# Optimization experiments

Hardware: AMD Instinct MI355X
Metric: run time of the kernel (lower is better)

The kernel has to match this reference:

```python
import jax, jax.numpy as jnp
import numpy as np

B, T, D, H, NH, E, K = 8, 1024, 512, 2048, 8, 8, 31
LN_EPS = 1e-12  # espnet LayerNorm default
BN_EPS = 1e-5


def setup_inputs() -> dict:
    key = jax.random.key(0)
    ks = iter(jax.random.split(key, 64))
    nrm = lambda shape, s=0.02: jax.random.normal(next(ks), shape, jnp.float32) * s
    return dict(
        x=jax.random.normal(next(ks), (B, T, D), jnp.float32),
        mask=jnp.ones((B, 1, T), bool),
        dialectid=jax.random.randint(next(ks), (B,), 1, E + 1),  # 1-based dialect ids
        ln_ffmac_g=jnp.ones((D,), jnp.float32), ln_ffmac_b=jnp.zeros((D,), jnp.float32),
        w1_mac=nrm((D, H)), b1_mac=jnp.zeros((H,), jnp.float32),
        w2_mac=nrm((H, D)), b2_mac=jnp.zeros((D,), jnp.float32),
        ln_mha_g=jnp.ones((D,), jnp.float32), ln_mha_b=jnp.zeros((D,), jnp.float32),
        wq=nrm((D, D)), bq=jnp.zeros((D,), jnp.float32),
        wk=nrm((D, D)), bk=jnp.zeros((D,), jnp.float32),
        wv=nrm((D, D)), bv=jnp.zeros((D,), jnp.float32),
        wo=nrm((D, D)), bo=jnp.zeros((D,), jnp.float32),
        ln_conv_g=jnp.ones((D,), jnp.float32), ln_conv_b=jnp.zeros((D,), jnp.float32),
        pw1_w=nrm((D, 2 * D)), pw1_b=jnp.zeros((2 * D,), jnp.float32),
        dw_w=nrm((D, 1, K)), dw_b=jnp.zeros((D,), jnp.float32),
        bn_g=jnp.ones((D,), jnp.float32), bn_b=jnp.zeros((D,), jnp.float32),
        bn_mean=jnp.zeros((D,), jnp.float32), bn_var=jnp.ones((D,), jnp.float32),
        pw2_w=nrm((D, D)), pw2_b=jnp.zeros((D,), jnp.float32),
        ln_ff_g=jnp.ones((D,), jnp.float32), ln_ff_b=jnp.zeros((D,), jnp.float32),
        gate_w=nrm((D, E)), gate_b=jnp.zeros((E,), jnp.float32),
        e_w1=nrm((E, D, H)), e_b1=jnp.zeros((E, H), jnp.float32),
        e_w2=nrm((E, H, D)), e_b2=jnp.zeros((E, D), jnp.float32),
        ln_final_g=jnp.ones((D,), jnp.float32), ln_final_b=jnp.zeros((D,), jnp.float32),
    )


def layer_norm(h, g, b):
    m = h.mean(-1, keepdims=True)
    v = ((h - m) ** 2).mean(-1, keepdims=True)
    return (h - m) * jax.lax.rsqrt(v + LN_EPS) * g + b


def mha(x, mask, wq, bq, wk, bk, wv, bv, wo, bo):
    dk = D // NH
    q = (x @ wq + bq).reshape(B, T, NH, dk)
    k = (x @ wk + bk).reshape(B, T, NH, dk)
    v = (x @ wv + bv).reshape(B, T, NH, dk)
    scores = jnp.einsum('bqhd,bkhd->bhqk', q, k) / jnp.sqrt(jnp.float32(dk))
    scores = jnp.where(mask[:, None, :, :], scores, jnp.float32(-1e9))  # [B,1,1,T] bcast
    attn = jax.nn.softmax(scores, axis=-1)
    o = jnp.einsum('bhqk,bkhd->bqhd', attn, v).reshape(B, T, D)
    return o @ wo + bo


def conv_module(x, pw1_w, pw1_b, dw_w, dw_b, bn_g, bn_b, bn_mean, bn_var, pw2_w, pw2_b):
    h = x @ pw1_w + pw1_b                                  # [B,T,2D]
    a, g = jnp.split(h, 2, axis=-1)
    h = a * jax.nn.sigmoid(g)                              # GLU -> [B,T,D]
    hc = jnp.transpose(h, (0, 2, 1))                       # [B,D,T]
    hc = jax.lax.conv_general_dilated(
        hc, dw_w, window_strides=(1,), padding=[(K // 2, K // 2)],
        dimension_numbers=('NCH', 'OIH', 'NCH'), feature_group_count=D)
    hc = hc + dw_b[None, :, None]
    h = jnp.transpose(hc, (0, 2, 1))                       # [B,T,D]
    h = (h - bn_mean) * jax.lax.rsqrt(bn_var + BN_EPS) * bn_g + bn_b  # BatchNorm (eval)
    h = h * jax.nn.sigmoid(h)                              # Swish
    return h @ pw2_w + pw2_b


def moe_ff(x, dialectid, gate_w, gate_b, e_w1, e_b1, e_w2, e_b2):
    probs = jax.nn.softmax(x.mean(1) @ gate_w + gate_b, axis=-1)   # [B,E]
    chosen = jnp.clip(dialectid - 1, 0, E - 1)                     # custom_expert_chosen
    w1 = e_w1[chosen]; b1 = e_b1[chosen]                           # gather [B,D,H]
    w2 = e_w2[chosen]; b2 = e_b2[chosen]
    h = jax.nn.relu(jnp.einsum('btd,bdh->bth', x, w1) + b1[:, None, :])
    y = jnp.einsum('bth,bhd->btd', h, w2) + b2[:, None, :]
    return y, probs, chosen


def reference(x, mask, dialectid,
              ln_ffmac_g, ln_ffmac_b, w1_mac, b1_mac, w2_mac, b2_mac,
              ln_mha_g, ln_mha_b, wq, bq, wk, bk, wv, bv, wo, bo,
              ln_conv_g, ln_conv_b, pw1_w, pw1_b, dw_w, dw_b,
              bn_g, bn_b, bn_mean, bn_var, pw2_w, pw2_b,
              ln_ff_g, ln_ff_b, gate_w, gate_b, e_w1, e_b1, e_w2, e_b2,
              ln_final_g, ln_final_b):
    ff_scale = 0.5  # macaron present
    # macaron feed-forward (pre-norm)
    residual = x
    h = layer_norm(x, ln_ffmac_g, ln_ffmac_b)
    h = jax.nn.relu(h @ w1_mac + b1_mac) @ w2_mac + b2_mac
    x = residual + ff_scale * h
    # self-attention
    residual = x
    h = layer_norm(x, ln_mha_g, ln_mha_b)
    x = residual + mha(h, mask, wq, bq, wk, bk, wv, bv, wo, bo)
    # convolution module
    residual = x
    h = layer_norm(x, ln_conv_g, ln_conv_b)
    x = residual + conv_module(h, pw1_w, pw1_b, dw_w, dw_b, bn_g, bn_b, bn_mean, bn_var, pw2_w, pw2_b)
    # MoE feed-forward
    residual = x
    h = layer_norm(x, ln_ff_g, ln_ff_b)
    h, expert_probs, expert_chosen = moe_ff(h, dialectid, gate_w, gate_b, e_w1, e_b1, e_w2, e_b2)
    x = residual + ff_scale * h
    # final norm (conv module present)
    x = layer_norm(x, ln_final_g, ln_final_b)
    return x
```

## Files before the change

### kernel.cpp

```cpp
#include <hip/hip_runtime.h>
#include <hip/hip_bf16.h>

constexpr int Bc = 8, Tc = 1024, Dc = 512, Hc = 2048, NHc = 8, DKc = 64, KC = 31;
constexpr long NTD = (long)Bc * Tc * Dc;

typedef short  bf16x8 __attribute__((ext_vector_type(8)));
typedef float  f32x4  __attribute__((ext_vector_type(4)));

__device__ __forceinline__ float bf2f(unsigned short u) {
  union { unsigned int i; float f; } c; c.i = ((unsigned int)u) << 16; return c.f;
}
__device__ __forceinline__ unsigned short f2bf(float f) {
  union { float f; unsigned int i; } c; c.f = f;
  unsigned int r = c.i + 0x7FFFu + ((c.i >> 16) & 1u);
  return (unsigned short)(r >> 16);
}
__device__ __forceinline__ float ldsc(const void* p, long i, int isbf) {
  return isbf ? bf2f(((const unsigned short*)p)[i]) : ((const float*)p)[i];
}
__device__ __forceinline__ void gl_lds16(const unsigned short* g, unsigned short* l) {
  __builtin_amdgcn_global_load_lds((const __attribute__((address_space(1))) void*)g,
                                   (__attribute__((address_space(3))) void*)l, 16, 0, 0);
}

__global__ void detect_k(const unsigned int* __restrict__ g, int* __restrict__ flag) {
  if (threadIdx.x == 0) flag[0] = (g[0] == 0x3F803F80u) ? 1 : 0;
}

__global__ __launch_bounds__(256) void cvt_k(const void* __restrict__ x,
                                             float* __restrict__ y, int n,
                                             const int* __restrict__ flag) {
  int isbf = flag[0];
  int i = blockIdx.x * 256 + threadIdx.x;
  if (i < n) y[i] = ldsc(x, i, isbf);
}

__global__ __launch_bounds__(256) void packb_k(const void* __restrict__ bq,
    const void* __restrict__ bk, const void* __restrict__ bv,
    float* __restrict__ o, const int* __restrict__ flag) {
  int isbf = flag[0];
  int i = blockIdx.x * 256 + threadIdx.x;
  const void* p = (i < 512) ? bq : ((i < 1024) ? bk : bv);
  o[i] = ldsc(p, i & 511, isbf);
}

__global__ __launch_bounds__(256) void transpose_k(const void* __restrict__ src_,
    unsigned short* __restrict__ dst, int K, int N,
    const int* __restrict__ dialectid, int batch0, const int* __restrict__ flag)
{
  int isbf = flag[0];
  long sofs = 0;
  if (dialectid) {
    int ex = dialectid[batch0 + blockIdx.z] - 1;
    ex = ex < 0 ? 0 : (ex > 7 ? 7 : ex);
    sofs = (long)ex * K * N;
    dst += (long)blockIdx.z * K * N;
  }
  __shared__ unsigned short t[32][36];
  int k0 = blockIdx.y * 32, n0 = blockIdx.x * 32;
  int r = threadIdx.x >> 3, c4 = (threadIdx.x & 7) * 4;
  long si = sofs + (long)(k0 + r) * N + n0 + c4;
  if (isbf) {
    ushort4 v = *reinterpret_cast<const ushort4*>((const unsigned short*)src_ + si);
    t[r][c4] = v.x; t[r][c4 + 1] = v.y; t[r][c4 + 2] = v.z; t[r][c4 + 3] = v.w;
  } else {
    float4 f = *reinterpret_cast<const float4*>((const float*)src_ + si);
    t[r][c4] = f2bf(f.x); t[r][c4 + 1] = f2bf(f.y);
    t[r][c4 + 2] = f2bf(f.z); t[r][c4 + 3] = f2bf(f.w);
  }
  __syncthreads();
  ushort4 o;
  o.x = t[c4 + 0][r]; o.y = t[c4 + 1][r]; o.z = t[c4 + 2][r]; o.w = t[c4 + 3][r];
  *reinterpret_cast<ushort4*>(dst + (long)(n0 + r) * K + k0 + c4) = o;
}

__global__ __launch_bounds__(256) void ln_k(const float* __restrict__ src,
    const void* __restrict__ g, const void* __restrict__ b,
    unsigned short* __restrict__ dst, const int* __restrict__ flag)
{
  int isbf = flag[0];
  int row = blockIdx.x;
  const float* p = src + (long)row * Dc;
  int tid = threadIdx.x;
  float x0 = p[tid], x1 = p[tid + 256];
  float s = x0 + x1, ss = x0 * x0 + x1 * x1;
#pragma unroll
  for (int off = 32; off; off >>= 1) { s += __shfl_xor(s, off); ss += __shfl_xor(ss, off); }
  __shared__ float rs[4], rss[4];
  int wave = tid >> 6, lane = tid & 63;
  if (lane == 0) { rs[wave] = s; rss[wave] = ss; }
  __syncthreads();
  s = rs[0] + rs[1] + rs[2] + rs[3];
  ss = rss[0] + rss[1] + rss[2] + rss[3];
  float mean = s * (1.0f / Dc);
  float var  = ss * (1.0f / Dc) - mean * mean;
  float inv  = rsqrtf(fmaxf(var, 0.0f) + 1e-12f);
  long base = (long)row * Dc;
  dst[base + tid]       = f2bf((x0 - mean) * inv * ldsc(g, tid, isbf)       + ldsc(b, tid, isbf));
  dst[base + tid + 256] = f2bf((x1 - mean) * inv * ldsc(g, tid + 256, isbf) + ldsc(b, tid + 256, isbf));
}

template<bool FINAL>
__global__ __launch_bounds__(256) void redln_k(float* x,
    const unsigned short* pb, long pplane, float scale,
    const void* __restrict__ g, const void* __restrict__ b,
    void* dst, const int* __restrict__ flag)
{
  int isbf = flag[0];
  int row = blockIdx.x;
  int tid = threadIdx.x;
  long base = (long)row * Dc;
  float x0 = x[base + tid]       + scale * (bf2f(pb[base + tid])       + bf2f(pb[pplane + base + tid]));
  float x1 = x[base + tid + 256] + scale * (bf2f(pb[base + tid + 256]) + bf2f(pb[pplane + base + tid + 256]));
  if (!FINAL) { x[base + tid] = x0; x[base + tid + 256] = x1; }
  float s = x0 + x1, ss = x0 * x0 + x1 * x1;
#pragma unroll
  for (int off = 32; off; off >>= 1) { s += __shfl_xor(s, off); ss += __shfl_xor(ss, off); }
  __shared__ float rs[4], rss[4];
  int wave = tid >> 6, lane = tid & 63;
  if (lane == 0) { rs[wave] = s; rss[wave] = ss; }
  __syncthreads();
  s = rs[0] + rs[1] + rs[2] + rs[3];
  ss = rss[0] + rss[1] + rss[2] + rss[3];
  float mean = s * (1.0f / Dc);
  float var  = ss * (1.0f / Dc) - mean * mean;
  float inv  = rsqrtf(fmaxf(var, 0.0f) + 1e-12f);
  float o0 = (x0 - mean) * inv * ldsc(g, tid, isbf)       + ldsc(b, tid, isbf);
  float o1 = (x1 - mean) * inv * ldsc(g, tid + 256, isbf) + ldsc(b, tid + 256, isbf);
  if (FINAL && !isbf) {
    ((float*)dst)[base + tid]       = o0;
    ((float*)dst)[base + tid + 256] = o1;
  } else {
    ((unsigned short*)dst)[base + tid]       = f2bf(o0);
    ((unsigned short*)dst)[base + tid + 256] = f2bf(o1);
  }
}

constexpr int EPI_STORE = 0, EPI_RELU = 1, EPI_ADD = 2, EPI_ADDHALF = 3,
              EPI_ROWDK = 4, EPI_DKROW = 5, EPI_ROWDK_Q = 6, EPI_QKV = 7,
              EPI_PART = 8;

template<int EPI, bool MOE, int SPLITK>
__global__ __launch_bounds__(256) void mgemm_k(
    const unsigned short* __restrict__ A,
    const unsigned short* __restrict__ BT,
    const void* __restrict__ bias,
    void* __restrict__ dst,
    int Kd, int N, const int* __restrict__ dialectid, int row_base,
    const int* __restrict__ flag, long pplane)
{
  int isbf = flag[0];
  __shared__ unsigned short As[3][128 * 32];
  __shared__ unsigned short Bs[3][128 * 32];
  int row0 = blockIdx.x * 128;
  int col0 = blockIdx.y * 128;
  const unsigned short* Bp = BT;
  long bofs = 0;
  if (MOE) {
    int bb = (row_base + row0) >> 10;
    int ex = dialectid[bb] - 1; ex = ex < 0 ? 0 : (ex > 7 ? 7 : ex);
    Bp += (long)(bb & 3) * (long)Kd * N;
    bofs = (long)ex * N;
  }
  int tid = threadIdx.x;
  int lane = tid & 63, wave = tid >> 6;
  int wm = (wave >> 1) * 64, wn = (wave & 1) * 64;
  int lm = lane & 15, quad = lane >> 4;
  int acol = ((lane & 3) ^ ((lane >> 3) & 3)) * 8;
  int rsl = (quad ^ ((lm >> 1) & 3)) * 8;

  f32x4 acc[4][4];
#pragma unroll
  for (int i = 0; i < 4; ++i)
#pragma unroll
    for (int j = 0; j < 4; ++j) acc[i][j] = (f32x4){0.f, 0.f, 0.f, 0.f};

  int kslice = Kd / SPLITK;
  int kbeg = (SPLITK > 1) ? (int)blockIdx.z * kslice : 0;
  int kend = kbeg + kslice;

  auto stage = [&](int buf, int k0) {
#pragma unroll
    for (int j = 0; j < 2; ++j) {
      int seg = wave * 2 + j;
      int r = seg * 16 + (lane >> 2);
      gl_lds16(A  + (long)(row0 + r) * Kd + k0 + acol, As[buf] + seg * 512);
      gl_lds16(Bp + (long)(col0 + r) * Kd + k0 + acol, Bs[buf] + seg * 512);
    }
  };

  stage(0, kbeg);
  if (kbeg + 32 < kend) {
    stage(1, kbeg + 32);
    asm volatile("s_waitcnt vmcnt(4)" ::: "memory");
  } else {
    asm volatile("s_waitcnt vmcnt(0)" ::: "memory");
  }
  __builtin_amdgcn_s_barrier();

  int cur = 0;
  for (int k0 = kbeg; k0 < kend; k0 += 32) {
    int pf = (k0 + 64 < kend);
    if (pf) {
      int nb = cur + 2; if (nb >= 3) nb -= 3;
      stage(nb, k0 + 64);
    }
    bf16x8 af[4], bfr[4];
#pragma unroll
    for (int t = 0; t < 4; ++t) {
      af[t]  = *reinterpret_cast<const bf16x8*>(As[cur] + (wm + t * 16 + lm) * 32 + rsl);
      bfr[t] = *reinterpret_cast<const bf16x8*>(Bs[cur] + (wn + t * 16 + lm) * 32 + rsl);
    }
    __builtin_amdgcn_s_setprio(1);
#pragma unroll
    for (int mt = 0; mt < 4; ++mt)
#pragma unroll
      for (int nt = 0; nt < 4; ++nt)
        acc[mt][nt] = __builtin_amdgcn_mfma_f32_16x16x32_bf16(af[mt], bfr[nt], acc[mt][nt], 0, 0, 0);
    __builtin_amdgcn_s_setprio(0);
    if (pf) asm volatile("s_waitcnt vmcnt(4)" ::: "memory");
    else    asm volatile("s_waitcnt vmcnt(0)" ::: "memory");
    __builtin_amdgcn_s_barrier();
    ++cur; if (cur >= 3) cur -= 3;
  }

  long zofs = (EPI == EPI_PART) ? (long)blockIdx.z * pplane : 0;
#pragma unroll
  for (int mt = 0; mt < 4; ++mt) {
#pragma unroll
    for (int nt = 0; nt < 4; ++nt) {
      int n = col0 + wn + nt * 16 + lm;
      float bv = (EPI == EPI_QKV) ? ((const float*)bias)[n]
                                  : ldsc(bias, bofs + n, isbf);
      if (SPLITK > 1 && blockIdx.z != 0) bv = 0.0f;
#pragma unroll
      for (int r = 0; r < 4; ++r) {
        int m = row0 + wm + mt * 16 + quad * 4 + r;
        float v = acc[mt][nt][r] + bv;
        if (EPI == EPI_STORE)
          ((unsigned short*)dst)[(long)m * N + n] = f2bf(v);
        else if (EPI == EPI_RELU)
          ((unsigned short*)dst)[(long)m * N + n] = f2bf(fmaxf(v, 0.0f));
        else if (EPI == EPI_PART)
          ((unsigned short*)dst)[zofs + (long)(row_base + m) * N + n] = f2bf(v);
        else if (EPI == EPI_ADD) {
          if (SPLITK == 1) ((float*)dst)[(long)m * N + n] += v;
          else             atomicAdd((float*)dst + ((long)m * N + n), v);
        } else if (EPI == EPI_ADDHALF) {
          if (SPLITK == 1) ((float*)dst)[(long)m * N + n] += 0.5f * v;
          else             atomicAdd((float*)dst + ((long)m * N + n), 0.5f * v);
        } else if (EPI == EPI_QKV) {
          int which = n >> 9, d = n & 511, hh = d >> 6, dd = d & 63;
          int bb = m >> 10, t = m & 1023;
          unsigned short* o = (unsigned short*)dst;
          if (which == 0)
            o[((long)(bb * NHc + hh) * Tc + t) * DKc + dd] = f2bf(v * 0.125f);
          else if (which == 1)
            o[4194304 + ((long)(bb * NHc + hh) * Tc + t) * DKc + dd] = f2bf(v);
          else
            o[8388608 + ((long)(bb * NHc + hh) * DKc + dd) * Tc + t] = f2bf(v);
        } else {
          int bb = m >> 10, t = m & 1023, hh = n >> 6, dd = n & 63;
          if (EPI == EPI_ROWDK)
            ((unsigned short*)dst)[((long)(bb * NHc + hh) * Tc + t) * DKc + dd] = f2bf(v);
          else if (EPI == EPI_ROWDK_Q)
            ((unsigned short*)dst)[((long)(bb * NHc + hh) * Tc + t) * DKc + dd] = f2bf(v * 0.125f);
          else
            ((unsigned short*)dst)[((long)(bb * NHc + hh) * DKc + dd) * Tc + t] = f2bf(v);
        }
      }
    }
  }
}

__global__ __launch_bounds__(256) void fattn_k(const unsigned short* __restrict__ q,
    const unsigned short* __restrict__ k, const unsigned short* __restrict__ vT,
    unsigned short* __restrict__ out)
{
  constexpr int PST = 72;
  __shared__ unsigned short ks[64 * PST];
  __shared__ unsigned short vs[64 * PST];
  __shared__ unsigned short plds[4][16][PST];
  int tid = threadIdx.x;
  int lane = tid & 63, wave = tid >> 6;
  int lm = lane & 15, quad = lane >> 4;
  int bh = blockIdx.y;
  int trow0 = blockIdx.x * 64 + wave * 16;
  long qbase = (long)bh * Tc * DKc;
  long vbase = (long)bh * DKc * Tc;

  int srow = tid >> 2, sseg = (tid & 3) * 16;

  bf16x8 aq[2];
#pragma unroll
  for (int s = 0; s < 2; ++s)
    aq[s] = *reinterpret_cast<const bf16x8*>(q + qbase + (long)(trow0 + lm) * DKc + s * 32 + quad * 8);

  f32x4 acc_o[4];
#pragma unroll
  for (int nt = 0; nt < 4; ++nt) acc_o[nt] = (f32x4){0.f, 0.f, 0.f, 0.f};
  float lsum[4] = {0.f, 0.f, 0.f, 0.f};

  float4 kr0 = *reinterpret_cast<const float4*>(k  + qbase + (long)srow * DKc + sseg);
  float4 kr1 = *reinterpret_cast<const float4*>(k  + qbase + (long)srow * DKc + sseg + 8);
  float4 vr0 = *reinterpret_cast<const float4*>(vT + vbase + (long)srow * Tc + sseg);
  float4 vr1 = *reinterpret_cast<const float4*>(vT + vbase + (long)srow * Tc + sseg + 8);

  for (int kt = 0; kt < Tc; kt += 64) {
    __syncthreads();
    *reinterpret_cast<float4*>(&ks[srow * PST + sseg])     = kr0;
    *reinterpret_cast<float4*>(&ks[srow * PST + sseg + 8]) = kr1;
    *reinterpret_cast<float4*>(&vs[srow * PST + sseg])     = vr0;
    *reinterpret_cast<float4*>(&vs[srow * PST + sseg + 8]) = vr1;
    __syncthreads();
    if (kt + 64 < Tc) {
      int kn = kt + 64;
      kr0 = *reinterpret_cast<const float4*>(k  + qbase + (long)(kn + srow) * DKc + sseg);
      kr1 = *reinterpret_cast<const float4*>(k  + qbase + (long)(kn + srow) * DKc + sseg + 8);
      vr0 = *reinterpret_cast<const float4*>(vT + vbase + (long)srow * Tc + kn + sseg);
      vr1 = *reinterpret_cast<const float4*>(vT + vbase + (long)srow * Tc + kn + sseg + 8);
    }
    f32x4 accs[4];
#pragma unroll
    for (int nt = 0; nt < 4; ++nt) accs[nt] = (f32x4){0.f, 0.f, 0.f, 0.f};
#pragma unroll
    for (int s = 0; s < 2; ++s) {
#pragma unroll
      for (int nt = 0; nt < 4; ++nt) {
        bf16x8 bk = *reinterpret_cast<const bf16x8*>(&ks[(nt * 16 + lm) * PST + s * 32 + quad * 8]);
        accs[nt] = __builtin_amdgcn_mfma_f32_16x16x32_bf16(aq[s], bk, accs[nt], 0, 0, 0);
      }
    }
#pragma unroll
    for (int nt = 0; nt < 4; ++nt) {
#pragma unroll
      for (int r = 0; r < 4; ++r) {
        float p = __expf(accs[nt][r]);
        lsum[r] += p;
        plds[wave][quad * 4 + r][nt * 16 + lm] = f2bf(p);
      }
    }
#pragma unroll
    for (int s = 0; s < 2; ++s) {
      bf16x8 ap = *reinterpret_cast<const bf16x8*>(&plds[wave][lm][s * 32 + quad * 8]);
#pragma unroll
      for (int nt = 0; nt < 4; ++nt) {
        bf16x8 bv = *reinterpret_cast<const bf16x8*>(&vs[(nt * 16 + lm) * PST + s * 32 + quad * 8]);
        acc_o[nt] = __builtin_amdgcn_mfma_f32_16x16x32_bf16(ap, bv, acc_o[nt], 0, 0, 0);
      }
    }
  }
  int bb = bh >> 3, hh = bh & 7;
#pragma unroll
  for (int r = 0; r < 4; ++r) {
    float l = lsum[r];
    l += __shfl_xor(l, 1);
    l += __shfl_xor(l, 2);
    l += __shfl_xor(l, 4);
    l += __shfl_xor(l, 8);
    float inv = 1.0f / l;
    int t = trow0 + quad * 4 + r;
#pragma unroll
    for (int nt = 0; nt < 4; ++nt)
      out[((long)(bb * Tc + t)) * Dc + hh * DKc + nt * 16 + lm] = f2bf(acc_o[nt][r] * inv);
  }
}

__global__ __launch_bounds__(256) void glu_k(const unsigned short* __restrict__ h,
                                             unsigned short* __restrict__ o) {
  int i = blockIdx.x * 256 + threadIdx.x;
  int m = i >> 9, d = i & 511;
  float a = bf2f(h[(long)m * 1024 + d]);
  float g = bf2f(h[(long)m * 1024 + 512 + d]);
  o[i] = f2bf(a * (1.0f / (1.0f + expf(-g))));
}

constexpr int TT = 16;
__global__ __launch_bounds__(256) void dwconv_k(const unsigned short* __restrict__ src,
    const void* __restrict__ w,  const void* __restrict__ wb,
    const void* __restrict__ bng, const void* __restrict__ bnb,
    const void* __restrict__ bnm, const void* __restrict__ bnv,
    unsigned short* __restrict__ dst, const int* __restrict__ flag)
{
  int isbf = flag[0];
  long i = (long)blockIdx.x * 256 + threadIdx.x;
  int d  = (int)(i & 511);
  int tc = (int)((i >> 9) & 63);
  int b  = (int)(i >> 15);
  int t0 = tc * TT;
  const unsigned short* s = src + (long)b * Tc * Dc + d;

  float win[TT + KC - 1];
#pragma unroll
  for (int j = 0; j < TT + KC - 1; ++j) {
    int tt = t0 + j - 15;
    win[j] = ((unsigned)tt < (unsigned)Tc) ? bf2f(s[(long)tt * Dc]) : 0.0f;
  }
  float wreg[KC];
#pragma unroll
  for (int kk = 0; kk < KC; ++kk) wreg[kk] = ldsc(w, d * KC + kk, isbf);

  float bias  = ldsc(wb, d, isbf);
  float scale = ldsc(bng, d, isbf) * rsqrtf(ldsc(bnv, d, isbf) + 1e-5f);
  float bnmv  = ldsc(bnm, d, isbf);
  float bnbv  = ldsc(bnb, d, isbf);
  unsigned short* o = dst + (long)b * Tc * Dc + (long)t0 * Dc + d;
#pragma unroll
  for (int r = 0; r < TT; ++r) {
    float acc = bias;
#pragma unroll
    for (int kk = 0; kk < KC; ++kk) acc += win[r + kk] * wreg[kk];
    float v = (acc - bnmv) * scale + bnbv;
    v = v * (1.0f / (1.0f + expf(-v)));
    o[(long)r * Dc] = f2bf(v);
  }
}

extern "C" void kernel_launch(void* const* d_in, const int* in_sizes, int n_in,
                              void* d_out, int out_size, void* d_ws, size_t ws_size,
                              hipStream_t stream) {
  const int* dialectid = (const int*)d_in[2];
  auto P = [&](int i) { return (const void*)d_in[i]; };

  char* base = (char*)d_ws;
  float*          x_cur = (float*)base;
  unsigned short* hn    = (unsigned short*)(base + (16L << 20));
  unsigned short* wt    = (unsigned short*)(base + (24L << 20));
  unsigned short* wtmoe = (unsigned short*)(base + (32L << 20));
  unsigned short* hidF  = (unsigned short*)(base + (32L << 20));
  unsigned short* dyn   = (unsigned short*)(base + (48L << 20));
  int*            flag  = (int*)(base + (72L << 20));
  unsigned short* w1T  = wt;
  unsigned short* w2T  = wt + 1048576;
  unsigned short* wqT  = wt + 2097152;
  unsigned short* wkT  = wt + 2359296;
  unsigned short* wvT  = wt + 2621440;
  unsigned short* woT  = wt + 2883584;
  unsigned short* pw1T = wt + 3145728;
  unsigned short* pw2T = wt + 3670016;
  float*          qkvb = (float*)(wt + 3932160);

  unsigned short* pbMac = hn;
  const long      ppMac = 25165824;
  unsigned short* pbDyn = dyn;
  const long      ppDyn = 4194304;
  unsigned short* pbMoE = wt;
  const long      ppMoE = 20971520;

  dim3 blk(256);
  const int nElem = (int)NTD;

  detect_k<<<1, 64, 0, stream>>>((const unsigned int*)d_in[3], flag);
  cvt_k<<<nElem / 256, blk, 0, stream>>>(P(0), x_cur, nElem, flag);

  transpose_k<<<dim3(64, 16), blk, 0, stream>>>(P(5),  w1T,  512, 2048, nullptr, 0, flag);
  transpose_k<<<dim3(16, 64), blk, 0, stream>>>(P(7),  w2T,  2048, 512, nullptr, 0, flag);
  transpose_k<<<dim3(16, 16), blk, 0, stream>>>(P(11), wqT,  512, 512,  nullptr, 0, flag);
  transpose_k<<<dim3(16, 16), blk, 0, stream>>>(P(13), wkT,  512, 512,  nullptr, 0, flag);
  transpose_k<<<dim3(16, 16), blk, 0, stream>>>(P(15), wvT,  512, 512,  nullptr, 0, flag);
  transpose_k<<<dim3(16, 16), blk, 0, stream>>>(P(17), woT,  512, 512,  nullptr, 0, flag);
  transpose_k<<<dim3(32, 16), blk, 0, stream>>>(P(21), pw1T, 512, 1024, nullptr, 0, flag);
  transpose_k<<<dim3(16, 16), blk, 0, stream>>>(P(29), pw2T, 512, 512,  nullptr, 0, flag);
  packb_k<<<6, blk, 0, stream>>>(P(12), P(14), P(16), qkvb, flag);

  unsigned short* hid = dyn;
  unsigned short* qb  = dyn;
  unsigned short* kb  = dyn + 4194304;
  unsigned short* vb  = dyn + 8388608;
  unsigned short* pw1o = dyn;
  unsigned short* gluo = dyn + 8388608;

  ln_k<<<Bc * Tc, blk, 0, stream>>>(x_cur, P(3), P(4), hn, flag);
  mgemm_k<EPI_RELU, false, 1><<<dim3(64, 16), blk, 0, stream>>>(
      hn, w1T, P(6), hidF, 512, 2048, nullptr, 0, flag, 0L);
  mgemm_k<EPI_PART, false, 2><<<dim3(64, 4, 2), blk, 0, stream>>>(
      hidF, w2T, P(8), pbMac, 2048, 512, nullptr, 0, flag, ppMac);
  redln_k<false><<<Bc * Tc, blk, 0, stream>>>(x_cur, pbMac, ppMac, 0.5f, P(9), P(10), hn, flag);

  mgemm_k<EPI_QKV, false, 1><<<dim3(64, 12), blk, 0, stream>>>(
      hn, wqT, qkvb, qb, 512, 1536, nullptr, 0, flag, 0L);
  fattn_k<<<dim3(Tc / 64, Bc * NHc), blk, 0, stream>>>(qb, kb, vb, hn);
  mgemm_k<EPI_PART, false, 2><<<dim3(64, 4, 2), blk, 0, stream>>>(
      hn, woT, P(18), pbDyn, 512, 512, nullptr, 0, flag, ppDyn);
  redln_k<false><<<Bc * Tc, blk, 0, stream>>>(x_cur, pbDyn, ppDyn, 1.0f, P(19), P(20), hn, flag);

  mgemm_k<EPI_STORE, false, 1><<<dim3(64, 8), blk, 0, stream>>>(hn, pw1T, P(22), pw1o, 512, 1024, nullptr, 0, flag, 0L);
  glu_k<<<nElem / 256, blk, 0, stream>>>(pw1o, gluo);
  dwconv_k<<<(int)(NTD / TT / 256), blk, 0, stream>>>(gluo, P(23), P(24), P(25), P(26), P(27), P(28), hn, flag);
  mgemm_k<EPI_PART, false, 2><<<dim3(64, 4, 2), blk, 0, stream>>>(
      hn, pw2T, P(30), pbDyn, 512, 512, nullptr, 0, flag, ppDyn);
  redln_k<false><<<Bc * Tc, blk, 0, stream>>>(x_cur, pbDyn, ppDyn, 1.0f, P(31), P(32), hn, flag);

  for (int c = 0; c < 2; ++c) {
    unsigned short* w1m = wtmoe;
    unsigned short* w2m = wtmoe + 4 * 1048576;
    transpose_k<<<dim3(64, 16, 4), blk, 0, stream>>>(P(35), w1m, 512, 2048, dialectid, c * 4, flag);
    transpose_k<<<dim3(16, 64, 4), blk, 0, stream>>>(P(37), w2m, 2048, 512, dialectid, c * 4, flag);
    mgemm_k<EPI_RELU, true, 1><<<dim3(32, 16), blk, 0, stream>>>(
        hn + (long)c * 4096 * 512, w1m, P(36), hid, 512, 2048, dialectid, c * 4096, flag, 0L);
    mgemm_k<EPI_PART, true, 2><<<dim3(32, 4, 2), blk, 0, stream>>>(
        hid, w2m, P(38), pbMoE, 2048, 512, dialectid, c * 4096, flag, ppMoE);
  }

  redln_k<true><<<Bc * Tc, blk, 0, stream>>>(x_cur, pbMoE, ppMoE, 0.5f, P(39), P(40), d_out, flag);
}
```

Baseline: 598.4 us.

## Process 32 query rows per wave in attention to reuse K/V tiles

Each wave in the attention kernel now handles two 16-row query tiles instead of one, so a block covers 128 query rows and every K/V tile staged in LDS feeds twice as many MFMAs. The grid shrinks from 1024 to 512 blocks and is flattened with a swizzle that places the 8 heads of one batch in consecutive block IDs. This halves K/V global loads and LDS staging per query row, but doubles accumulator registers and the P scratch buffer, which may reduce occupancy and leave fewer blocks to spread across CUs.

```diff
diff --git a/kernel.cpp b/kernel.cpp
--- a/kernel.cpp
+++ b/kernel.cpp
@@ -280,26 +280,33 @@
   constexpr int PST = 72;
   __shared__ unsigned short ks[64 * PST];
   __shared__ unsigned short vs[64 * PST];
-  __shared__ unsigned short plds[4][16][PST];
+  __shared__ unsigned short plds[4][32][PST];
   int tid = threadIdx.x;
   int lane = tid & 63, wave = tid >> 6;
   int lm = lane & 15, quad = lane >> 4;
-  int bh = blockIdx.y;
-  int trow0 = blockIdx.x * 64 + wave * 16;
+  int flat = blockIdx.x;
+  int bh = ((flat >> 6) << 3) | (flat & 7);
+  int qt = (flat >> 3) & 7;
+  int trow0 = qt * 128 + wave * 32;
   long qbase = (long)bh * Tc * DKc;
   long vbase = (long)bh * DKc * Tc;
 
   int srow = tid >> 2, sseg = (tid & 3) * 16;
 
-  bf16x8 aq[2];
-#pragma unroll
-  for (int s = 0; s < 2; ++s)
-    aq[s] = *reinterpret_cast<const bf16x8*>(q + qbase + (long)(trow0 + lm) * DKc + s * 32 + quad * 8);
-
-  f32x4 acc_o[4];
-#pragma unroll
-  for (int nt = 0; nt < 4; ++nt) acc_o[nt] = (f32x4){0.f, 0.f, 0.f, 0.f};
-  float lsum[4] = {0.f, 0.f, 0.f, 0.f};
+  bf16x8 aq[2][2];
+#pragma unroll
+  for (int mt = 0; mt < 2; ++mt)
+#pragma unroll
+    for (int s = 0; s < 2; ++s)
+      aq[mt][s] = *reinterpret_cast<const bf16x8*>(
+          q + qbase + (long)(trow0 + mt * 16 + lm) * DKc + s * 32 + quad * 8);
+
+  f32x4 acc_o[2][4];
+#pragma unroll
+  for (int mt = 0; mt < 2; ++mt)
+#pragma unroll
+    for (int nt = 0; nt < 4; ++nt) acc_o[mt][nt] = (f32x4){0.f, 0.f, 0.f, 0.f};
+  float lsum[2][4] = {{0.f, 0.f, 0.f, 0.f}, {0.f, 0.f, 0.f, 0.f}};
 
   float4 kr0 = *reinterpret_cast<const float4*>(k  + qbase + (long)srow * DKc + sseg);
   float4 kr1 = *reinterpret_cast<const float4*>(k  + qbase + (long)srow * DKc + sseg + 8);
@@ -320,49 +327,60 @@
       vr0 = *reinterpret_cast<const float4*>(vT + vbase + (long)srow * Tc + kn + sseg);
       vr1 = *reinterpret_cast<const float4*>(vT + vbase + (long)srow * Tc + kn + sseg + 8);
     }
-    f32x4 accs[4];
-#pragma unroll
-    for (int nt = 0; nt < 4; ++nt) accs[nt] = (f32x4){0.f, 0.f, 0.f, 0.f};
+    f32x4 accs[2][4];
+#pragma unroll
+    for (int mt = 0; mt < 2; ++mt)
+#pragma unroll
+      for (int nt = 0; nt < 4; ++nt) accs[mt][nt] = (f32x4){0.f, 0.f, 0.f, 0.f};
 #pragma unroll
     for (int s = 0; s < 2; ++s) {
 #pragma unroll
       for (int nt = 0; nt < 4; ++nt) {
         bf16x8 bk = *reinterpret_cast<const bf16x8*>(&ks[(nt * 16 + lm) * PST + s * 32 + quad * 8]);
-        accs[nt] = __builtin_amdgcn_mfma_f32_16x16x32_bf16(aq[s], bk, accs[nt], 0, 0, 0);
+#pragma unroll
+        for (int mt = 0; mt < 2; ++mt)
+          accs[mt][nt] = __builtin_amdgcn_mfma_f32_16x16x32_bf16(aq[mt][s], bk, accs[mt][nt], 0, 0, 0);
       }
     }
 #pragma unroll
-    for (int nt = 0; nt < 4; ++nt) {
-#pragma unroll
-      for (int r = 0; r < 4; ++r) {
-        float p = __expf(accs[nt][r]);
-        lsum[r] += p;
-        plds[wave][quad * 4 + r][nt * 16 + lm] = f2bf(p);
+    for (int mt = 0; mt < 2; ++mt)
+#pragma unroll
+      for (int nt = 0; nt < 4; ++nt) {
+#pragma unroll
+        for (int r = 0; r < 4; ++r) {
+          float p = __expf(accs[mt][nt][r]);
+          lsum[mt][r] += p;
+          plds[wave][mt * 16 + quad * 4 + r][nt * 16 + lm] = f2bf(p);
+        }
       }
-    }
 #pragma unroll
     for (int s = 0; s < 2; ++s) {
-      bf16x8 ap = *reinterpret_cast<const bf16x8*>(&plds[wave][lm][s * 32 + quad * 8]);
+      bf16x8 ap0 = *reinterpret_cast<const bf16x8*>(&plds[wave][lm][s * 32 + quad * 8]);
+      bf16x8 ap1 = *reinterpret_cast<const bf16x8*>(&plds[wave][16 + lm][s * 32 + quad * 8]);
 #pragma unroll
       for (int nt = 0; nt < 4; ++nt) {
         bf16x8 bv = *reinterpret_cast<const bf16x8*>(&vs[(nt * 16 + lm) * PST + s * 32 + quad * 8]);
-        acc_o[nt] = __builtin_amdgcn_mfma_f32_16x16x32_bf16(ap, bv, acc_o[nt], 0, 0, 0);
+        acc_o[0][nt] = __builtin_amdgcn_mfma_f32_16x16x32_bf16(ap0, bv, acc_o[0][nt], 0, 0, 0);
+        acc_o[1][nt] = __builtin_amdgcn_mfma_f32_16x16x32_bf16(ap1, bv, acc_o[1][nt], 0, 0, 0);
       }
     }
   }
   int bb = bh >> 3, hh = bh & 7;
 #pragma unroll
-  for (int r = 0; r < 4; ++r) {
-    float l = lsum[r];
-    l += __shfl_xor(l, 1);
-    l += __shfl_xor(l, 2);
-    l += __shfl_xor(l, 4);
-    l += __shfl_xor(l, 8);
-    float inv = 1.0f / l;
-    int t = trow0 + quad * 4 + r;
-#pragma unroll
-    for (int nt = 0; nt < 4; ++nt)
-      out[((long)(bb * Tc + t)) * Dc + hh * DKc + nt * 16 + lm] = f2bf(acc_o[nt][r] * inv);
+  for (int mt = 0; mt < 2; ++mt) {
+#pragma unroll
+    for (int r = 0; r < 4; ++r) {
+      float l = lsum[mt][r];
+      l += __shfl_xor(l, 1);
+      l += __shfl_xor(l, 2);
+      l += __shfl_xor(l, 4);
+      l += __shfl_xor(l, 8);
+      float inv = 1.0f / l;
+      int t = trow0 + mt * 16 + quad * 4 + r;
+#pragma unroll
+      for (int nt = 0; nt < 4; ++nt)
+        out[((long)(bb * Tc + t)) * Dc + hh * DKc + nt * 16 + lm] = f2bf(acc_o[mt][nt][r] * inv);
+    }
   }
 }
 
@@ -479,7 +497,7 @@
 
   mgemm_k<EPI_QKV, false, 1><<<dim3(64, 12), blk, 0, stream>>>(
       hn, wqT, qkvb, qb, 512, 1536, nullptr, 0, flag, 0L);
-  fattn_k<<<dim3(Tc / 64, Bc * NHc), blk, 0, stream>>>(qb, kb, vb, hn);
+  fattn_k<<<dim3(512), blk, 0, stream>>>(qb, kb, vb, hn);
   mgemm_k<EPI_PART, false, 2><<<dim3(64, 4, 2), blk, 0, stream>>>(
       hn, woT, P(18), pbDyn, 512, 512, nullptr, 0, flag, ppDyn);
   redln_k<false><<<Bc * Tc, blk, 0, stream>>>(x_cur, pbDyn, ppDyn, 1.0f, P(19), P(20), hn, flag);
```

New measurement: 600.9 us. Within noise of the previous version (+0.4%).
